# Kernel tuning notes

Measured on AMD Instinct MI355X. Metric: run time of the kernel, lower is better.

Reference implementation:

```python
import jax, jax.numpy as jnp
import numpy as np

EPS = 1e-5

def layer_norm(x, gamma, beta):
    mu = jnp.mean(x, axis=-1, keepdims=True)
    var = jnp.mean(jnp.square(x - mu), axis=-1, keepdims=True)
    return (x - mu) * jax.lax.rsqrt(var + EPS) * gamma + beta

def setup_inputs() -> dict:
    key = jax.random.key(0)
    ks = jax.random.split(key, 10)
    B, I, H = 4096, 2048, 2048
    G = 4 * H
    s_ih = 1.0 / np.sqrt(I)
    s_hh = 1.0 / np.sqrt(H)
    b_ih = jax.random.uniform(ks[4], (G,), jnp.float32, -s_ih, s_ih)
    b_hh = jax.random.uniform(ks[5], (G,), jnp.float32, -s_hh, s_hh)
    # forget-gate bias init to 1.0 (slot [H:2H] per the torch code's chunk order)
    b_ih = b_ih.at[H:2*H].set(1.0)
    b_hh = b_hh.at[H:2*H].set(1.0)
    return {
        "x": jax.random.normal(ks[0], (B, I), jnp.float32),
        "h_prev": jax.random.normal(ks[1], (B, H), jnp.float32),
        "c_prev": jax.random.normal(ks[2], (B, H), jnp.float32),
        "W_ih": jax.random.normal(ks[3], (I, G), jnp.float32) * s_ih,
        "W_hh": jax.random.normal(ks[6], (H, G), jnp.float32) * s_hh,
        "b_ih": b_ih,
        "b_hh": b_hh,
        "g_x": jnp.ones((G,), jnp.float32),
        "beta_x": jnp.zeros((G,), jnp.float32),
        "g_c": jnp.ones((H,), jnp.float32),
        "beta_c": jnp.zeros((H,), jnp.float32),
        "g_h": jnp.ones((H,), jnp.float32),
        "beta_h": jnp.zeros((H,), jnp.float32),
    }

def reference(x, h_prev, c_prev, W_ih, W_hh, b_ih, b_hh, g_x, beta_x, g_c, beta_c, g_h, beta_h):
    gates_x = layer_norm(x @ W_ih + b_ih, g_x, beta_x)   # LN only on input-path gates
    gates = gates_x + (h_prev @ W_hh + b_hh)              # [B, 4H]
    i_g, f_g, gg, o_g = jnp.split(gates, 4, axis=1)
    i_t = jax.nn.sigmoid(i_g)
    f_t = jax.nn.sigmoid(f_g)
    g_t = jnp.tanh(gg)
    o_t = jax.nn.sigmoid(o_g)
    c_t = layer_norm(f_t * c_prev + i_t * g_t, g_c, beta_c)
    h_t = layer_norm(o_t * jnp.tanh(c_t), g_h, beta_h)
    return (h_t, c_t)
```

## Files before the change

### kernel.cpp

```cpp
#include <hip/hip_runtime.h>
#include <stdint.h>

typedef unsigned short ushort_t;
typedef __attribute__((ext_vector_type(8))) short short8;
typedef __attribute__((ext_vector_type(4))) float f32x4;
typedef __attribute__((ext_vector_type(4))) ushort_t u16x4;

#define M_ROWS 4096
#define K_DIM  2048
#define N_GATE 8192
#define H_DIM  2048

__device__ __forceinline__ ushort_t f2bf(float f) {
    uint32_t u = __float_as_uint(f);
    uint32_t r = (u + 0x7FFFu + ((u >> 16) & 1u)) >> 16;
    return (ushort_t)r;
}
__device__ __forceinline__ float bf2f(ushort_t b) {
    return __uint_as_float(((uint32_t)b) << 16);
}
__device__ __forceinline__ float sigf(float x) {
    return 1.0f / (1.0f + __expf(-x));
}
__device__ __forceinline__ float tanh_fast(float x) {
    float e = __expf(2.0f * x);
    return 1.0f - 2.0f / (e + 1.0f);
}

__global__ void cvt2_f32_bf16(const float* __restrict__ in0, ushort_t* __restrict__ out0,
                              const float* __restrict__ in1, ushort_t* __restrict__ out1, int n) {
    const float* in  = blockIdx.y ? in1 : in0;
    ushort_t*    out = blockIdx.y ? out1 : out0;
    int i = (blockIdx.x * blockDim.x + threadIdx.x) * 4;
    if (i >= n) return;
    float4 v = *(const float4*)(in + i);
    u16x4 o;
    o[0] = f2bf(v.x); o[1] = f2bf(v.y); o[2] = f2bf(v.z); o[3] = f2bf(v.w);
    *(u16x4*)(out + i) = o;
}

__global__ void transpose_cvt2(const float* __restrict__ W0, ushort_t* __restrict__ Wt0,
                               const float* __restrict__ W1, ushort_t* __restrict__ Wt1,
                               int K, int N) {
    const float* W  = blockIdx.z ? W1 : W0;
    ushort_t*    Wt = blockIdx.z ? Wt1 : Wt0;
    __shared__ float tile[32][33];
    int bn = blockIdx.x * 32;
    int bk = blockIdx.y * 32;
    int tx = threadIdx.x;
    int ty = threadIdx.y;
#pragma unroll
    for (int i = 0; i < 32; i += 8)
        tile[ty + i][tx] = W[(size_t)(bk + ty + i) * N + bn + tx];
    __syncthreads();
#pragma unroll
    for (int i = 0; i < 32; i += 8)
        Wt[(size_t)(bn + ty + i) * K + bk + tx] = f2bf(tile[tx][ty + i]);
}

#define TBK 64

__global__ __launch_bounds__(512, 2) void gemm256_8ph(
    const ushort_t* __restrict__ A0, const ushort_t* __restrict__ B0, ushort_t* __restrict__ C0,
    const ushort_t* __restrict__ A1, const ushort_t* __restrict__ B1, ushort_t* __restrict__ C1,
    int M, int N, int K) {
    extern __shared__ char smem[];
    const ushort_t* A  = blockIdx.z ? A1 : A0;
    const ushort_t* Bt = blockIdx.z ? B1 : B0;
    ushort_t*       C  = blockIdx.z ? C1 : C0;

    const int t    = threadIdx.x;
    const int lane = t & 63, wid = t >> 6;
    const int wm   = wid >> 2, wn = wid & 3;
    const int l15  = lane & 15;
    const int l4c  = (lane >> 4) * 16;

    const int linear = blockIdx.y * gridDim.x + blockIdx.x;
    const int swz    = (linear & 7) * (int)((gridDim.x * gridDim.y) >> 3) + (linear >> 3);
    const int brow = (swz >> 5) * 256;
    const int bcol = (swz & 31) * 256;

    const int srow = t >> 3;
    const int scol = (((t & 7) ^ ((t >> 3) & 7)) * 8);
    const ushort_t* gA = A  + (size_t)(brow + srow) * K + scol;
    const ushort_t* gB = Bt + (size_t)(bcol + srow) * K + scol;
    const int ldsw = wid * 1024;

    int aR[4], abit[4], bR[2], bbit[2];
#pragma unroll
    for (int fm = 0; fm < 4; ++fm) { int r = wm * 64 + fm * 16 + l15; aR[fm] = r * 128; abit[fm] = (r & 7) << 4; }
#pragma unroll
    for (int fn = 0; fn < 2; ++fn) { int r = wn * 32 + fn * 16 + l15; bR[fn] = r * 128; bbit[fn] = (r & 7) << 4; }

    f32x4 acc[8][4];
#pragma unroll
    for (int i = 0; i < 8; ++i)
#pragma unroll
        for (int j = 0; j < 4; ++j) acc[i][j] = f32x4{0.f, 0.f, 0.f, 0.f};

    short8 a[4][2], b0[2][2], b1[2][2];

#define STAGE_A(tt, h, buf) { _Pragma("unroll") for (int j = 0; j < 2; ++j) \
    __builtin_amdgcn_global_load_lds( \
        (const __attribute__((address_space(1))) void*)(gA + ((size_t)((h) * 128 + j * 64)) * K + (size_t)(tt) * TBK), \
        (__attribute__((address_space(3))) void*)(smem + (buf) * 65536 + (h) * 16384 + j * 8192 + ldsw), 16, 0, 0); }
#define STAGE_B(tt, h, buf) { _Pragma("unroll") for (int j = 0; j < 2; ++j) \
    __builtin_amdgcn_global_load_lds( \
        (const __attribute__((address_space(1))) void*)(gB + ((size_t)((h) * 128 + j * 64)) * K + (size_t)(tt) * TBK), \
        (__attribute__((address_space(3))) void*)(smem + 32768 + (buf) * 65536 + (h) * 16384 + j * 8192 + ldsw), 16, 0, 0); }
#define LDA(mh, buf) { _Pragma("unroll") for (int fm = 0; fm < 4; ++fm) _Pragma("unroll") for (int ks = 0; ks < 2; ++ks) \
    a[fm][ks] = *(const short8*)(smem + (buf) * 65536 + (mh) * 16384 + aR[fm] + ((ks * 64 + l4c) ^ abit[fm])); }
#define LDB(dst, nh, buf) { _Pragma("unroll") for (int fn = 0; fn < 2; ++fn) _Pragma("unroll") for (int ks = 0; ks < 2; ++ks) \
    dst[fn][ks] = *(const short8*)(smem + 32768 + (buf) * 65536 + (nh) * 16384 + bR[fn] + ((ks * 64 + l4c) ^ bbit[fn])); }
#define BARRIER() __builtin_amdgcn_s_barrier()
#define LGKM0()  { asm volatile("s_waitcnt lgkmcnt(0)" ::: "memory"); __builtin_amdgcn_sched_barrier(0); }
#define VM6()    asm volatile("s_waitcnt vmcnt(6)" ::: "memory")
#define MM(mh, nh, bb) { __builtin_amdgcn_s_setprio(1); \
    _Pragma("unroll") for (int ks = 0; ks < 2; ++ks) \
    _Pragma("unroll") for (int fm = 0; fm < 4; ++fm) \
    _Pragma("unroll") for (int fn = 0; fn < 2; ++fn) \
        acc[(mh) * 4 + fm][(nh) * 2 + fn] = __builtin_amdgcn_mfma_f32_16x16x32_bf16( \
            a[fm][ks], bb[fn][ks], acc[(mh) * 4 + fm][(nh) * 2 + fn], 0, 0, 0); \
    __builtin_amdgcn_s_setprio(0); }

    STAGE_A(0, 0, 0); STAGE_B(0, 0, 0); STAGE_B(0, 1, 0); STAGE_A(0, 1, 0);
    STAGE_A(1, 0, 1); STAGE_B(1, 0, 1); STAGE_B(1, 1, 1);
    VM6();
    BARRIER();

    const int NT = K / TBK;
    for (int tt = 0; tt < NT; tt += 2) {
        const int s2 = (tt + 2) & (NT - 1);
        const int s3 = (tt + 3) & (NT - 1);
        LDA(0, 0); LDB(b0, 0, 0);
        STAGE_A(tt + 1, 1, 1);
        BARRIER(); LGKM0(); MM(0, 0, b0); BARRIER();
        LDB(b1, 1, 0);
        STAGE_A(s2, 0, 0);
        BARRIER(); LGKM0(); MM(0, 1, b1); BARRIER();
        LDA(1, 0);
        STAGE_B(s2, 0, 0);
        BARRIER(); LGKM0(); MM(1, 0, b0); BARRIER();
        STAGE_B(s2, 1, 0);
        VM6();
        BARRIER(); LGKM0(); MM(1, 1, b1); BARRIER();
        LDA(0, 1); LDB(b0, 0, 1);
        STAGE_A(s2, 1, 0);
        BARRIER(); LGKM0(); MM(0, 0, b0); BARRIER();
        LDB(b1, 1, 1);
        STAGE_A(s3, 0, 1);
        BARRIER(); LGKM0(); MM(0, 1, b1); BARRIER();
        LDA(1, 1);
        STAGE_B(s3, 0, 1);
        BARRIER(); LGKM0(); MM(1, 0, b0); BARRIER();
        STAGE_B(s3, 1, 1);
        VM6();
        BARRIER(); LGKM0(); MM(1, 1, b1); BARRIER();
    }

    asm volatile("s_waitcnt vmcnt(0)" ::: "memory");
    BARRIER();
#pragma unroll
    for (int i = 0; i < 8; ++i) {
        const int mh = i >> 2, fm = i & 3;
        const int rbase = mh * 128 + wm * 64 + fm * 16 + (lane >> 4) * 4;
#pragma unroll
        for (int jn = 0; jn < 4; ++jn) {
            const int nh = jn >> 1, fn = jn & 1;
            const int colb = (nh * 128 + wn * 32 + fn * 16 + l15) * 2;
#pragma unroll
            for (int r = 0; r < 4; ++r) {
                const int row = rbase + r;
                *(ushort_t*)(smem + row * 512 + (colb ^ ((row & 7) << 4))) = f2bf(acc[i][jn][r]);
            }
        }
    }
    BARRIER();
    {
        const int row   = t >> 1;
        const int halfb = (t & 1) * 256;
        ushort_t* gout = C + (size_t)(brow + row) * N + bcol + (t & 1) * 128;
#pragma unroll
        for (int c = 0; c < 16; ++c)
            *(short8*)(gout + c * 8) =
                *(const short8*)(smem + row * 512 + ((halfb + c * 16) ^ ((row & 7) << 4)));
    }
#undef STAGE_A
#undef STAGE_B
#undef LDA
#undef LDB
#undef BARRIER
#undef LGKM0
#undef VM6
#undef MM
}

__device__ __forceinline__ void block_reduce2(float& a, float& b, float* sred, int t) {
#pragma unroll
    for (int o = 32; o; o >>= 1) {
        a += __shfl_down(a, o);
        b += __shfl_down(b, o);
    }
    __syncthreads();
    if ((t & 63) == 0) { int w = t >> 6; sred[w] = a; sred[4 + w] = b; }
    __syncthreads();
    a = sred[0] + sred[1] + sred[2] + sred[3];
    b = sred[4] + sred[5] + sred[6] + sred[7];
}

__global__ __launch_bounds__(256) void fuse_ln_lstm(
    const ushort_t* __restrict__ xW, const ushort_t* __restrict__ hW,
    const float* __restrict__ c_prev,
    const float* __restrict__ b_ih, const float* __restrict__ b_hh,
    const float* __restrict__ g_x, const float* __restrict__ beta_x,
    const float* __restrict__ g_c, const float* __restrict__ beta_c,
    const float* __restrict__ g_h, const float* __restrict__ beta_h,
    float* __restrict__ h_out, float* __restrict__ c_out) {

    __shared__ float sgx[N_GATE];
    __shared__ float scell[H_DIM];
    __shared__ float sot[H_DIM];
    __shared__ float sred[8];

    const int b = blockIdx.x;
    const int t = threadIdx.x;
    const ushort_t* xwr = xW + (size_t)b * N_GATE;
    const ushort_t* hwr = hW + (size_t)b * N_GATE;
    const float*    cpr = c_prev + (size_t)b * H_DIM;

    float s = 0.f, q = 0.f;
#pragma unroll
    for (int it = 0; it < 4; ++it) {
        int idx = it * 2048 + t * 8;
        short8 v = *(const short8*)&xwr[idx];
#pragma unroll
        for (int j = 0; j < 8; ++j) {
            float f = bf2f((ushort_t)v[j]) + b_ih[idx + j];
            sgx[idx + j] = f;
            s += f; q += f * f;
        }
    }
    block_reduce2(s, q, sred, t);
    const float inv_g = 1.0f / (float)N_GATE;
    float mu   = s * inv_g;
    float rstd = rsqrtf(q * inv_g - mu * mu + 1e-5f);

    float cs = 0.f, cq = 0.f;
#pragma unroll
    for (int it = 0; it < 8; ++it) {
        int j = it * 256 + t;
        int ji = j, jf = j + 2048, jg = j + 4096, jo = j + 6144;
        float gi = (sgx[ji] - mu) * rstd * g_x[ji] + beta_x[ji] + bf2f(hwr[ji]) + b_hh[ji];
        float gf = (sgx[jf] - mu) * rstd * g_x[jf] + beta_x[jf] + bf2f(hwr[jf]) + b_hh[jf];
        float gg = (sgx[jg] - mu) * rstd * g_x[jg] + beta_x[jg] + bf2f(hwr[jg]) + b_hh[jg];
        float go = (sgx[jo] - mu) * rstd * g_x[jo] + beta_x[jo] + bf2f(hwr[jo]) + b_hh[jo];
        float i_t = sigf(gi);
        float f_t = sigf(gf);
        float g_t = tanh_fast(gg);
        float o_t = sigf(go);
        float cell = f_t * cpr[j] + i_t * g_t;
        scell[j] = cell;
        sot[j]   = o_t;
        cs += cell; cq += cell * cell;
    }
    block_reduce2(cs, cq, sred, t);
    const float inv_h = 1.0f / (float)H_DIM;
    float muc   = cs * inv_h;
    float rstdc = rsqrtf(cq * inv_h - muc * muc + 1e-5f);

    float hs = 0.f, hq = 0.f;
#pragma unroll
    for (int it = 0; it < 8; ++it) {
        int j = it * 256 + t;
        float ct = (scell[j] - muc) * rstdc * g_c[j] + beta_c[j];
        c_out[(size_t)b * H_DIM + j] = ct;
        float hp = sot[j] * tanh_fast(ct);
        sgx[j] = hp;
        hs += hp; hq += hp * hp;
    }
    block_reduce2(hs, hq, sred, t);
    float muh   = hs * inv_h;
    float rstdh = rsqrtf(hq * inv_h - muh * muh + 1e-5f);

#pragma unroll
    for (int it = 0; it < 8; ++it) {
        int j = it * 256 + t;
        h_out[(size_t)b * H_DIM + j] = (sgx[j] - muh) * rstdh * g_h[j] + beta_h[j];
    }
}

extern "C" void kernel_launch(void* const* d_in, const int* in_sizes, int n_in,
                              void* d_out, int out_size, void* d_ws, size_t ws_size,
                              hipStream_t stream) {
    const float* x      = (const float*)d_in[0];
    const float* h_prev = (const float*)d_in[1];
    const float* c_prev = (const float*)d_in[2];
    const float* W_ih   = (const float*)d_in[3];
    const float* W_hh   = (const float*)d_in[4];
    const float* b_ih   = (const float*)d_in[5];
    const float* b_hh   = (const float*)d_in[6];
    const float* g_x    = (const float*)d_in[7];
    const float* beta_x = (const float*)d_in[8];
    const float* g_c    = (const float*)d_in[9];
    const float* beta_c = (const float*)d_in[10];
    const float* g_h    = (const float*)d_in[11];
    const float* beta_h = (const float*)d_in[12];

    const int M = M_ROWS, K = K_DIM, N = N_GATE;

    ushort_t* Xb   = (ushort_t*)d_ws;
    ushort_t* Hb   = Xb   + (size_t)M * K;
    ushort_t* WihT = Hb   + (size_t)M * K;
    ushort_t* WhhT = WihT + (size_t)N * K;
    ushort_t* xWb  = WhhT + (size_t)N * K;
    ushort_t* hWb  = xWb  + (size_t)M * N;

    const int n_xh = M * K;
    cvt2_f32_bf16<<<dim3(n_xh / (256 * 4), 2), 256, 0, stream>>>(x, Xb, h_prev, Hb, n_xh);

    transpose_cvt2<<<dim3(N / 32, K / 32, 2), dim3(32, 8), 0, stream>>>(
        W_ih, WihT, W_hh, WhhT, K, N);

    static int lds_attr_set = 0;
    if (!lds_attr_set) {
        (void)hipFuncSetAttribute(reinterpret_cast<const void*>(&gemm256_8ph),
                                  hipFuncAttributeMaxDynamicSharedMemorySize, 131072);
        lds_attr_set = 1;
    }
    gemm256_8ph<<<dim3(N / 256, M / 256, 2), 512, 131072, stream>>>(
        Xb, WihT, xWb, Hb, WhhT, hWb, M, N, K);

    float* h_out = (float*)d_out;
    float* c_out = h_out + (size_t)M * H_DIM;
    fuse_ln_lstm<<<M, 256, 0, stream>>>(xWb, hWb, c_prev, b_ih, b_hh,
                                        g_x, beta_x, g_c, beta_c, g_h, beta_h,
                                        h_out, c_out);
}
```

Baseline: 393.0 us.

## Vectorize conversion, transpose and LSTM epilogue; drop GEMM block swizzle

The fp32-to-bf16 conversion now handles 8 elements per thread. The weight transpose moves to 64x64 tiles with float4 loads and 16-byte bf16 stores. The fused LN-LSTM kernel gives each thread 8 contiguous columns held in registers, so the shared-memory cell and output-gate buffers go away and all global parameter loads and stores are vectorized. Separately, the GEMM's L2-oriented block-index swizzle is replaced by a plain row-major block mapping, which may reduce cache reuse of the A and B tiles.

```diff
diff --git a/kernel.cpp b/kernel.cpp
--- a/kernel.cpp
+++ b/kernel.cpp
@@ -3,8 +3,8 @@
 
 typedef unsigned short ushort_t;
 typedef __attribute__((ext_vector_type(8))) short short8;
+typedef __attribute__((ext_vector_type(8))) ushort_t u16x8;
 typedef __attribute__((ext_vector_type(4))) float f32x4;
-typedef __attribute__((ext_vector_type(4))) ushort_t u16x4;
 
 #define M_ROWS 4096
 #define K_DIM  2048
@@ -27,35 +27,52 @@
     return 1.0f - 2.0f / (e + 1.0f);
 }
 
-__global__ void cvt2_f32_bf16(const float* __restrict__ in0, ushort_t* __restrict__ out0,
-                              const float* __restrict__ in1, ushort_t* __restrict__ out1, int n) {
+__global__ __launch_bounds__(256) void cvt2_f32_bf16(
+    const float* __restrict__ in0, ushort_t* __restrict__ out0,
+    const float* __restrict__ in1, ushort_t* __restrict__ out1, int n) {
     const float* in  = blockIdx.y ? in1 : in0;
     ushort_t*    out = blockIdx.y ? out1 : out0;
-    int i = (blockIdx.x * blockDim.x + threadIdx.x) * 4;
+    int i = (blockIdx.x * 256 + threadIdx.x) * 8;
     if (i >= n) return;
-    float4 v = *(const float4*)(in + i);
-    u16x4 o;
-    o[0] = f2bf(v.x); o[1] = f2bf(v.y); o[2] = f2bf(v.z); o[3] = f2bf(v.w);
-    *(u16x4*)(out + i) = o;
-}
-
-__global__ void transpose_cvt2(const float* __restrict__ W0, ushort_t* __restrict__ Wt0,
-                               const float* __restrict__ W1, ushort_t* __restrict__ Wt1,
-                               int K, int N) {
+    float4 a = *(const float4*)(in + i);
+    float4 b = *(const float4*)(in + i + 4);
+    u16x8 o;
+    o[0] = f2bf(a.x); o[1] = f2bf(a.y); o[2] = f2bf(a.z); o[3] = f2bf(a.w);
+    o[4] = f2bf(b.x); o[5] = f2bf(b.y); o[6] = f2bf(b.z); o[7] = f2bf(b.w);
+    *(u16x8*)(out + i) = o;
+}
+
+__global__ __launch_bounds__(256) void transpose_cvt2(
+    const float* __restrict__ W0, ushort_t* __restrict__ Wt0,
+    const float* __restrict__ W1, ushort_t* __restrict__ Wt1,
+    int K, int N) {
     const float* W  = blockIdx.z ? W1 : W0;
     ushort_t*    Wt = blockIdx.z ? Wt1 : Wt0;
-    __shared__ float tile[32][33];
-    int bn = blockIdx.x * 32;
-    int bk = blockIdx.y * 32;
-    int tx = threadIdx.x;
-    int ty = threadIdx.y;
-#pragma unroll
-    for (int i = 0; i < 32; i += 8)
-        tile[ty + i][tx] = W[(size_t)(bk + ty + i) * N + bn + tx];
+    __shared__ float tile[64][65];
+    const int bn = blockIdx.x * 64;
+    const int bk = blockIdx.y * 64;
+    const int tr = threadIdx.x >> 4;
+    const int tc = (threadIdx.x & 15) * 4;
+#pragma unroll
+    for (int i = 0; i < 64; i += 16) {
+        float4 v = *(const float4*)&W[(size_t)(bk + tr + i) * N + bn + tc];
+        tile[tr + i][tc]     = v.x;
+        tile[tr + i][tc + 1] = v.y;
+        tile[tr + i][tc + 2] = v.z;
+        tile[tr + i][tc + 3] = v.w;
+    }
     __syncthreads();
-#pragma unroll
-    for (int i = 0; i < 32; i += 8)
-        Wt[(size_t)(bn + ty + i) * K + bk + tx] = f2bf(tile[tx][ty + i]);
+    const int n0 = threadIdx.x >> 3;
+    const int k0 = (threadIdx.x & 7) * 8;
+#pragma unroll
+    for (int p = 0; p < 2; ++p) {
+        const int n = n0 + p * 32;
+        u16x8 o;
+#pragma unroll
+        for (int j = 0; j < 8; ++j)
+            o[j] = f2bf(tile[k0 + j][n]);
+        *(u16x8*)&Wt[(size_t)(bn + n) * K + bk + k0] = o;
+    }
 }
 
 #define TBK 64
@@ -75,10 +92,8 @@
     const int l15  = lane & 15;
     const int l4c  = (lane >> 4) * 16;
 
-    const int linear = blockIdx.y * gridDim.x + blockIdx.x;
-    const int swz    = (linear & 7) * (int)((gridDim.x * gridDim.y) >> 3) + (linear >> 3);
-    const int brow = (swz >> 5) * 256;
-    const int bcol = (swz & 31) * 256;
+    const int brow = blockIdx.y * 256;
+    const int bcol = blockIdx.x * 256;
 
     const int srow = t >> 3;
     const int scol = (((t & 7) ^ ((t >> 3) & 7)) * 8);
@@ -218,8 +233,6 @@
     float* __restrict__ h_out, float* __restrict__ c_out) {
 
     __shared__ float sgx[N_GATE];
-    __shared__ float scell[H_DIM];
-    __shared__ float sot[H_DIM];
     __shared__ float sred[8];
 
     const int b = blockIdx.x;
@@ -233,9 +246,12 @@
     for (int it = 0; it < 4; ++it) {
         int idx = it * 2048 + t * 8;
         short8 v = *(const short8*)&xwr[idx];
+        float bi[8];
+        *(float4*)&bi[0] = *(const float4*)&b_ih[idx];
+        *(float4*)&bi[4] = *(const float4*)&b_ih[idx + 4];
 #pragma unroll
         for (int j = 0; j < 8; ++j) {
-            float f = bf2f((ushort_t)v[j]) + b_ih[idx + j];
+            float f = bf2f((ushort_t)v[j]) + bi[j];
             sgx[idx + j] = f;
             s += f; q += f * f;
         }
@@ -245,48 +261,66 @@
     float mu   = s * inv_g;
     float rstd = rsqrtf(q * inv_g - mu * mu + 1e-5f);
 
+    const int j0 = t * 8;
+    float gi[8], gf[8], gg[8], go[8];
+#define GATE(dst, off) { \
+    const int jj = j0 + (off); \
+    short8 hv = *(const short8*)&hwr[jj]; \
+    float bh[8], gx[8], bx[8]; \
+    *(float4*)&bh[0] = *(const float4*)&b_hh[jj];   *(float4*)&bh[4] = *(const float4*)&b_hh[jj + 4]; \
+    *(float4*)&gx[0] = *(const float4*)&g_x[jj];    *(float4*)&gx[4] = *(const float4*)&g_x[jj + 4]; \
+    *(float4*)&bx[0] = *(const float4*)&beta_x[jj]; *(float4*)&bx[4] = *(const float4*)&beta_x[jj + 4]; \
+    _Pragma("unroll") for (int u = 0; u < 8; ++u) \
+        dst[u] = (sgx[jj + u] - mu) * rstd * gx[u] + bx[u] + bf2f((ushort_t)hv[u]) + bh[u]; }
+    GATE(gi, 0); GATE(gf, 2048); GATE(gg, 4096); GATE(go, 6144);
+#undef GATE
+    float cp[8];
+    *(float4*)&cp[0] = *(const float4*)&cpr[j0];
+    *(float4*)&cp[4] = *(const float4*)&cpr[j0 + 4];
+    float cell[8], ot[8];
     float cs = 0.f, cq = 0.f;
 #pragma unroll
-    for (int it = 0; it < 8; ++it) {
-        int j = it * 256 + t;
-        int ji = j, jf = j + 2048, jg = j + 4096, jo = j + 6144;
-        float gi = (sgx[ji] - mu) * rstd * g_x[ji] + beta_x[ji] + bf2f(hwr[ji]) + b_hh[ji];
-        float gf = (sgx[jf] - mu) * rstd * g_x[jf] + beta_x[jf] + bf2f(hwr[jf]) + b_hh[jf];
-        float gg = (sgx[jg] - mu) * rstd * g_x[jg] + beta_x[jg] + bf2f(hwr[jg]) + b_hh[jg];
-        float go = (sgx[jo] - mu) * rstd * g_x[jo] + beta_x[jo] + bf2f(hwr[jo]) + b_hh[jo];
-        float i_t = sigf(gi);
-        float f_t = sigf(gf);
-        float g_t = tanh_fast(gg);
-        float o_t = sigf(go);
-        float cell = f_t * cpr[j] + i_t * g_t;
-        scell[j] = cell;
-        sot[j]   = o_t;
-        cs += cell; cq += cell * cell;
+    for (int u = 0; u < 8; ++u) {
+        float i_t = sigf(gi[u]);
+        float f_t = sigf(gf[u]);
+        float g_t = tanh_fast(gg[u]);
+        ot[u]     = sigf(go[u]);
+        cell[u]   = f_t * cp[u] + i_t * g_t;
+        cs += cell[u]; cq += cell[u] * cell[u];
     }
     block_reduce2(cs, cq, sred, t);
     const float inv_h = 1.0f / (float)H_DIM;
     float muc   = cs * inv_h;
     float rstdc = rsqrtf(cq * inv_h - muc * muc + 1e-5f);
 
+    float gc[8], bc[8];
+    *(float4*)&gc[0] = *(const float4*)&g_c[j0];    *(float4*)&gc[4] = *(const float4*)&g_c[j0 + 4];
+    *(float4*)&bc[0] = *(const float4*)&beta_c[j0]; *(float4*)&bc[4] = *(const float4*)&beta_c[j0 + 4];
+    float ct[8], hp[8];
     float hs = 0.f, hq = 0.f;
 #pragma unroll
-    for (int it = 0; it < 8; ++it) {
-        int j = it * 256 + t;
-        float ct = (scell[j] - muc) * rstdc * g_c[j] + beta_c[j];
-        c_out[(size_t)b * H_DIM + j] = ct;
-        float hp = sot[j] * tanh_fast(ct);
-        sgx[j] = hp;
-        hs += hp; hq += hp * hp;
-    }
+    for (int u = 0; u < 8; ++u) {
+        ct[u] = (cell[u] - muc) * rstdc * gc[u] + bc[u];
+        hp[u] = ot[u] * tanh_fast(ct[u]);
+        hs += hp[u]; hq += hp[u] * hp[u];
+    }
+    float* cout = c_out + (size_t)b * H_DIM + j0;
+    *(float4*)&cout[0] = *(const float4*)&ct[0];
+    *(float4*)&cout[4] = *(const float4*)&ct[4];
     block_reduce2(hs, hq, sred, t);
     float muh   = hs * inv_h;
     float rstdh = rsqrtf(hq * inv_h - muh * muh + 1e-5f);
 
-#pragma unroll
-    for (int it = 0; it < 8; ++it) {
-        int j = it * 256 + t;
-        h_out[(size_t)b * H_DIM + j] = (sgx[j] - muh) * rstdh * g_h[j] + beta_h[j];
-    }
+    float gh[8], bh2[8];
+    *(float4*)&gh[0]  = *(const float4*)&g_h[j0];    *(float4*)&gh[4]  = *(const float4*)&g_h[j0 + 4];
+    *(float4*)&bh2[0] = *(const float4*)&beta_h[j0]; *(float4*)&bh2[4] = *(const float4*)&beta_h[j0 + 4];
+    float ho[8];
+#pragma unroll
+    for (int u = 0; u < 8; ++u)
+        ho[u] = (hp[u] - muh) * rstdh * gh[u] + bh2[u];
+    float* hout = h_out + (size_t)b * H_DIM + j0;
+    *(float4*)&hout[0] = *(const float4*)&ho[0];
+    *(float4*)&hout[4] = *(const float4*)&ho[4];
 }
 
 extern "C" void kernel_launch(void* const* d_in, const int* in_sizes, int n_in,
@@ -316,9 +350,9 @@
     ushort_t* hWb  = xWb  + (size_t)M * N;
 
     const int n_xh = M * K;
-    cvt2_f32_bf16<<<dim3(n_xh / (256 * 4), 2), 256, 0, stream>>>(x, Xb, h_prev, Hb, n_xh);
-
-    transpose_cvt2<<<dim3(N / 32, K / 32, 2), dim3(32, 8), 0, stream>>>(
+    cvt2_f32_bf16<<<dim3(n_xh / (256 * 8), 2), 256, 0, stream>>>(x, Xb, h_prev, Hb, n_xh);
+
+    transpose_cvt2<<<dim3(N / 64, K / 64, 2), 256, 0, stream>>>(
         W_ih, WihT, W_hh, WhhT, K, N);
 
     static int lds_attr_set = 0;
```

After: 393.9 us. Within noise of the previous version (+0.2%).
